# Kernel optimization log

Hardware: AMD Instinct MI355X
Metric: run time of the kernel (lower is better)

Reference implementation:

```python
import jax, jax.numpy as jnp
import numpy as np

N = 100000   # nodes
E = 3200000  # directed edges
EPS = 1e-5   # batchnorm eps


def setup_inputs() -> dict:
    key = jax.random.key(0)
    ks = jax.random.split(key, 12)
    x = jax.random.normal(ks[0], (N, 128), jnp.float32)
    edge_index = jax.random.randint(ks[1], (2, E), 0, N, dtype=jnp.int32).astype(jnp.int64)
    W1 = jax.random.normal(ks[2], (128, 256), jnp.float32) * (1.0 / np.sqrt(128))
    W2 = jax.random.normal(ks[3], (256, 256), jnp.float32) * (1.0 / np.sqrt(256))
    W3 = jax.random.normal(ks[4], (256, 40), jnp.float32) * (1.0 / np.sqrt(256))
    return {
        "x": x, "edge_index": edge_index,
        "W1": W1, "b1": jnp.zeros((256,), jnp.float32),
        "W2": W2, "b2": jnp.zeros((256,), jnp.float32),
        "W3": W3, "b3": jnp.zeros((40,), jnp.float32),
        "g1": jnp.ones((256,), jnp.float32), "be1": jnp.zeros((256,), jnp.float32),
        "g2": jnp.ones((256,), jnp.float32), "be2": jnp.zeros((256,), jnp.float32),
    }


def _gcn_conv(x, src, dst, norm, W, b):
    # GCNConv: transform then normalized sparse aggregation (A_hat @ (x W)) + b
    h = x @ W                              # [N, F_out]
    msg = h[src] * norm[:, None]           # gather + edge scaling, [E+N, F_out]
    return jax.ops.segment_sum(msg, dst, num_segments=N) + b


def _bn(h, g, b):
    # BatchNorm over the node dimension (batch stats, biased variance)
    m = h.mean(axis=0)
    v = h.var(axis=0)
    return (h - m) * jax.lax.rsqrt(v + EPS) * g + b


def reference(x, edge_index, W1, b1, W2, b2, W3, b3, g1, be1, g2, be2):
    # add self-loops (A + I), symmetric degree normalization D^-1/2 (A+I) D^-1/2
    loop = jnp.arange(N, dtype=edge_index.dtype)
    src = jnp.concatenate([edge_index[0], loop])
    dst = jnp.concatenate([edge_index[1], loop])
    deg = jax.ops.segment_sum(jnp.ones_like(src, jnp.float32), dst, num_segments=N)
    dinv = jax.lax.rsqrt(jnp.maximum(deg, 1.0))
    norm = dinv[src] * dinv[dst]           # [E+N]

    h = _gcn_conv(x, src, dst, norm, W1, b1)
    h = jax.nn.relu(_bn(h, g1, be1))       # dropout: identity (eval mode)
    h = _gcn_conv(h, src, dst, norm, W2, b2)
    h = jax.nn.relu(_bn(h, g2, be2))
    h = _gcn_conv(h, src, dst, norm, W3, b3)
    return jax.nn.log_softmax(h, axis=1)
```

## Files before the change

kernel.cpp:

```cpp
#include <hip/hip_runtime.h>
#include <hip/hip_bf16.h>
#include <math.h>

#define NNODES 100000
#define NEDGES 3200000
#define BN_EPS 1e-5f
#define NCH 391

typedef unsigned int uint;
typedef unsigned short ushort;
typedef __attribute__((ext_vector_type(8))) short bf16x8;
typedef __attribute__((ext_vector_type(4))) float f32x4;

__device__ inline float bflo(uint u) { return __uint_as_float(u << 16); }
__device__ inline float bfhi(uint u) { return __uint_as_float(u & 0xffff0000u); }
__device__ inline ushort f2bf(float f) {
    __hip_bfloat16 h = __float2bfloat16(f);
    union { __hip_bfloat16 b; ushort u; } c; c.b = h; return c.u;
}


__global__ void k_hist(const int* __restrict__ dst, int* __restrict__ cnt) {
    int e = (blockIdx.x * 256 + threadIdx.x) * 2;
    int2 v = *(const int2*)(dst + e);
    atomicAdd(&cnt[v.x], 1);
    atomicAdd(&cnt[v.y], 1);
}

__global__ void k_deg(const int* __restrict__ cnt, float* __restrict__ dinv,
                      int* __restrict__ chunksums) {
    __shared__ int s[256];
    int i = blockIdx.x * 256 + threadIdx.x;
    int c = (i < NNODES) ? cnt[i] : 0;
    if (i < NNODES) dinv[i] = rsqrtf((float)c + 1.0f);
    s[threadIdx.x] = c;
    __syncthreads();
    for (int o = 128; o > 0; o >>= 1) {
        if (threadIdx.x < o) s[threadIdx.x] += s[threadIdx.x + o];
        __syncthreads();
    }
    if (threadIdx.x == 0) chunksums[blockIdx.x] = s[0];
}

__global__ void k_scan1(int* __restrict__ chunksums, int* __restrict__ rowstart) {
    __shared__ int s[512];
    int t = threadIdx.x;
    int v = (t < NCH) ? chunksums[t] : 0;
    s[t] = v;
    __syncthreads();
    for (int o = 1; o < 512; o <<= 1) {
        int add = (t >= o) ? s[t - o] : 0;
        __syncthreads();
        s[t] += add;
        __syncthreads();
    }
    if (t < NCH) chunksums[t] = s[t] - v;
    if (t == NCH - 1) rowstart[NNODES] = s[t];
}

__global__ void k_scan2(const int* __restrict__ cnt, const int* __restrict__ chunkbase,
                        int* __restrict__ rowstart, int* __restrict__ cursor) {
    __shared__ int s[256];
    int t = threadIdx.x;
    int i = blockIdx.x * 256 + t;
    int v = (i < NNODES) ? cnt[i] : 0;
    s[t] = v;
    __syncthreads();
    for (int o = 1; o < 256; o <<= 1) {
        int add = (t >= o) ? s[t - o] : 0;
        __syncthreads();
        s[t] += add;
        __syncthreads();
    }
    if (i < NNODES) {
        int excl = s[t] - v + chunkbase[blockIdx.x];
        rowstart[i] = excl;
        cursor[i]   = excl;
    }
}

__global__ void k_scatter(const int* __restrict__ src, const int* __restrict__ dst,
                          const float* __restrict__ dinv, int* __restrict__ cursor,
                          int2* __restrict__ pairs) {
    int e = blockIdx.x * 256 + threadIdx.x;
    if (e >= NEDGES) return;
    int s = src[e], d = dst[e];
    int p = atomicAdd(&cursor[d], 1);
    float w = dinv[s] * dinv[d];
    pairs[p] = make_int2(s, __float_as_int(w));
}


template <int F, int U>
__global__ __launch_bounds__(256) void k_aggh(
    const ushort* __restrict__ X, ushort* __restrict__ Y,
    const int2* __restrict__ pairs, const int* __restrict__ rowstart,
    const float* __restrict__ dinv) {
    constexpr int CPL = F / 32;
    const int wv = threadIdx.x >> 6;
    const int lane = threadIdx.x & 63;
    const int h = lane >> 5, l32 = lane & 31;
    const int d = blockIdx.x * 4 + wv;
    const int r0 = rowstart[d], r1 = rowstart[d + 1];
    const ushort* Xb = X + (size_t)CPL * l32;
    float acc[CPL] = {};
    int p = r0;
    for (; p + 2 * U <= r1; p += 2 * U) {
        int2 e[U];
#pragma unroll
        for (int j = 0; j < U; ++j) e[j] = pairs[p + 2 * j + h];
        if constexpr (CPL == 8) {
            uint4 u[U];
#pragma unroll
            for (int j = 0; j < U; ++j) u[j] = *(const uint4*)(Xb + (size_t)e[j].x * F);
#pragma unroll
            for (int j = 0; j < U; ++j) {
                float w = __int_as_float(e[j].y);
                acc[0]=fmaf(w,bflo(u[j].x),acc[0]); acc[1]=fmaf(w,bfhi(u[j].x),acc[1]);
                acc[2]=fmaf(w,bflo(u[j].y),acc[2]); acc[3]=fmaf(w,bfhi(u[j].y),acc[3]);
                acc[4]=fmaf(w,bflo(u[j].z),acc[4]); acc[5]=fmaf(w,bfhi(u[j].z),acc[5]);
                acc[6]=fmaf(w,bflo(u[j].w),acc[6]); acc[7]=fmaf(w,bfhi(u[j].w),acc[7]);
            }
        } else {
            uint2 u[U];
#pragma unroll
            for (int j = 0; j < U; ++j) u[j] = *(const uint2*)(Xb + (size_t)e[j].x * F);
#pragma unroll
            for (int j = 0; j < U; ++j) {
                float w = __int_as_float(e[j].y);
                acc[0]=fmaf(w,bflo(u[j].x),acc[0]); acc[1]=fmaf(w,bfhi(u[j].x),acc[1]);
                acc[2]=fmaf(w,bflo(u[j].y),acc[2]); acc[3]=fmaf(w,bfhi(u[j].y),acc[3]);
            }
        }
    }
    for (; p + 2 <= r1; p += 2) {
        int2 e = pairs[p + h];
        float w = __int_as_float(e.y);
        if constexpr (CPL == 8) {
            uint4 u = *(const uint4*)(Xb + (size_t)e.x * F);
            acc[0]=fmaf(w,bflo(u.x),acc[0]); acc[1]=fmaf(w,bfhi(u.x),acc[1]);
            acc[2]=fmaf(w,bflo(u.y),acc[2]); acc[3]=fmaf(w,bfhi(u.y),acc[3]);
            acc[4]=fmaf(w,bflo(u.z),acc[4]); acc[5]=fmaf(w,bfhi(u.z),acc[5]);
            acc[6]=fmaf(w,bflo(u.w),acc[6]); acc[7]=fmaf(w,bfhi(u.w),acc[7]);
        } else {
            uint2 u = *(const uint2*)(Xb + (size_t)e.x * F);
            acc[0]=fmaf(w,bflo(u.x),acc[0]); acc[1]=fmaf(w,bfhi(u.x),acc[1]);
            acc[2]=fmaf(w,bflo(u.y),acc[2]); acc[3]=fmaf(w,bfhi(u.y),acc[3]);
        }
    }
    if (p < r1 && h == 0) {
        int2 e = pairs[p];
        float w = __int_as_float(e.y);
        if constexpr (CPL == 8) {
            uint4 u = *(const uint4*)(Xb + (size_t)e.x * F);
            acc[0]=fmaf(w,bflo(u.x),acc[0]); acc[1]=fmaf(w,bfhi(u.x),acc[1]);
            acc[2]=fmaf(w,bflo(u.y),acc[2]); acc[3]=fmaf(w,bfhi(u.y),acc[3]);
            acc[4]=fmaf(w,bflo(u.z),acc[4]); acc[5]=fmaf(w,bfhi(u.z),acc[5]);
            acc[6]=fmaf(w,bflo(u.w),acc[6]); acc[7]=fmaf(w,bfhi(u.w),acc[7]);
        } else {
            uint2 u = *(const uint2*)(Xb + (size_t)e.x * F);
            acc[0]=fmaf(w,bflo(u.x),acc[0]); acc[1]=fmaf(w,bfhi(u.x),acc[1]);
            acc[2]=fmaf(w,bflo(u.y),acc[2]); acc[3]=fmaf(w,bfhi(u.y),acc[3]);
        }
    }
#pragma unroll
    for (int c = 0; c < CPL; ++c) acc[c] += __shfl_xor(acc[c], 32);
    if (h == 0) {
        float di = dinv[d], ws = di * di;
        if constexpr (CPL == 8) {
            uint4 u = *(const uint4*)(Xb + (size_t)d * F);
            acc[0]=fmaf(ws,bflo(u.x),acc[0]); acc[1]=fmaf(ws,bfhi(u.x),acc[1]);
            acc[2]=fmaf(ws,bflo(u.y),acc[2]); acc[3]=fmaf(ws,bfhi(u.y),acc[3]);
            acc[4]=fmaf(ws,bflo(u.z),acc[4]); acc[5]=fmaf(ws,bfhi(u.z),acc[5]);
            acc[6]=fmaf(ws,bflo(u.w),acc[6]); acc[7]=fmaf(ws,bfhi(u.w),acc[7]);
            uint4 o;
            o.x = (uint)f2bf(acc[0]) | ((uint)f2bf(acc[1]) << 16);
            o.y = (uint)f2bf(acc[2]) | ((uint)f2bf(acc[3]) << 16);
            o.z = (uint)f2bf(acc[4]) | ((uint)f2bf(acc[5]) << 16);
            o.w = (uint)f2bf(acc[6]) | ((uint)f2bf(acc[7]) << 16);
            *(uint4*)(Y + (size_t)d * F + CPL * l32) = o;
        } else {
            uint2 u = *(const uint2*)(Xb + (size_t)d * F);
            acc[0]=fmaf(ws,bflo(u.x),acc[0]); acc[1]=fmaf(ws,bfhi(u.x),acc[1]);
            acc[2]=fmaf(ws,bflo(u.y),acc[2]); acc[3]=fmaf(ws,bfhi(u.y),acc[3]);
            uint2 o;
            o.x = (uint)f2bf(acc[0]) | ((uint)f2bf(acc[1]) << 16);
            o.y = (uint)f2bf(acc[2]) | ((uint)f2bf(acc[3]) << 16);
            *(uint2*)(Y + (size_t)d * F + CPL * l32) = o;
        }
    }
}


__global__ __launch_bounds__(256) void k_agg40lsm(
    const ushort* __restrict__ X, float* __restrict__ out,
    const int2* __restrict__ pairs, const int* __restrict__ rowstart,
    const float* __restrict__ dinv, const float* __restrict__ bias) {
    int t = threadIdx.x;
    int wid = t >> 6, lane = t & 63;
    int sub = lane >> 5, l32 = lane & 31;
    int d = blockIdx.x * 8 + wid * 2 + sub;
    bool act = l32 < 20;
    int col = act ? 2 * l32 : 0;
    const int r0 = rowstart[d], r1 = rowstart[d + 1];
    float a0 = 0.f, a1 = 0.f;
    int p = r0;
    for (; p + 8 <= r1; p += 8) {
        int2 e[8]; uint u[8];
#pragma unroll
        for (int j = 0; j < 8; ++j) e[j] = pairs[p + j];
#pragma unroll
        for (int j = 0; j < 8; ++j) u[j] = *(const uint*)(X + (size_t)e[j].x * 40 + col);
#pragma unroll
        for (int j = 0; j < 8; ++j) {
            float w = __int_as_float(e[j].y);
            a0 = fmaf(w, bflo(u[j]), a0); a1 = fmaf(w, bfhi(u[j]), a1);
        }
    }
    for (; p < r1; ++p) {
        int2 e = pairs[p];
        uint u = *(const uint*)(X + (size_t)e.x * 40 + col);
        float w_ = __int_as_float(e.y);
        a0 = fmaf(w_, bflo(u), a0); a1 = fmaf(w_, bfhi(u), a1);
    }
    float di = dinv[d], ws = di * di;
    uint us = *(const uint*)(X + (size_t)d * 40 + col);
    a0 = fmaf(ws, bflo(us), a0); a1 = fmaf(ws, bfhi(us), a1);
    if (act) { a0 += bias[col]; a1 += bias[col + 1]; }
    else     { a0 = -INFINITY;  a1 = -INFINITY; }
    float mx = fmaxf(a0, a1);
    for (int o = 16; o > 0; o >>= 1) mx = fmaxf(mx, __shfl_xor(mx, o, 32));
    float e = act ? (expf(a0 - mx) + expf(a1 - mx)) : 0.f;
    float s = e;
    for (int o = 16; o > 0; o >>= 1) s += __shfl_xor(s, o, 32);
    float ls = logf(s);
    if (act)
        *(float2*)(out + (size_t)d * 40 + col) = make_float2(a0 - mx - ls, a1 - mx - ls);
}


__global__ void k_xtobf16(const float* __restrict__ X, ushort* __restrict__ O) {
    int i = blockIdx.x * 256 + threadIdx.x;
    float4 v = ((const float4*)X)[i];
    ushort4 o; o.x=f2bf(v.x); o.y=f2bf(v.y); o.z=f2bf(v.z); o.w=f2bf(v.w);
    ((ushort4*)O)[i] = o;
}

__global__ void k_wconv3(const float* __restrict__ W1, const float* __restrict__ W2,
                         const float* __restrict__ W3, ushort* __restrict__ W1t,
                         ushort* __restrict__ W2t, ushort* __restrict__ W3t) {
    int b = blockIdx.x;
    if (b < 256) {
        int n = b;
        for (int k = threadIdx.x; k < 128; k += 256)
            W1t[n * 128 + k] = f2bf(W1[(size_t)k * 256 + n]);
    } else if (b < 512) {
        int n = b - 256;
        for (int k = threadIdx.x; k < 256; k += 256)
            W2t[n * 256 + k] = f2bf(W2[(size_t)k * 256 + n]);
    } else {
        int n = b - 512;
        for (int k = threadIdx.x; k < 256; k += 256)
            W3t[n * 256 + k] = (n < 40) ? f2bf(W3[(size_t)k * 40 + n]) : (ushort)0;
    }
}


__device__ inline bf16x8 bnrelu8(bf16x8 v, const float* __restrict__ scsh, int ch) {
    bf16x8 r;
#pragma unroll
    for (int j = 0; j < 8; ++j) {
        float f = __uint_as_float(((uint)(ushort)v[j]) << 16);
        f = fmaxf(fmaf(f, scsh[ch + j], scsh[256 + ch + j]), 0.f);
        r[j] = (short)f2bf(f);
    }
    return r;
}

template <int K, bool BNA, bool STATS>
__global__ __launch_bounds__(256) void k_gmm(
    const ushort* __restrict__ A, const ushort* __restrict__ Bt,
    const float* __restrict__ scsh, ushort* __restrict__ C,
    float* __restrict__ sums) {
    __shared__ ushort As[128 * 32];
    __shared__ ushort Bs[128 * 32];
    const int m0 = blockIdx.x * 128;
    const int n0 = blockIdx.y * 128;
    const int tid = threadIdx.x;
    const int lane = tid & 63;
    const int wid = tid >> 6;
    const int wr = wid >> 1, wc = wid & 1;
    const int sr1 = tid >> 2, sc = tid & 3;
    const int sr2 = sr1 + 64;
    const int ssl1 = sr1 * 32 + ((sc ^ ((sr1 >> 1) & 3)) * 8);
    const int ssl2 = sr2 * 32 + ((sc ^ ((sr2 >> 1) & 3)) * 8);
    const size_t ga1 = (size_t)min(m0 + sr1, NNODES - 1) * K + sc * 8;
    const size_t ga2 = (size_t)min(m0 + sr2, NNODES - 1) * K + sc * 8;
    const size_t gb1 = (size_t)(n0 + sr1) * K + sc * 8;
    const size_t gb2 = (size_t)(n0 + sr2) * K + sc * 8;
    const int kc = lane >> 4, rr = lane & 15;
    f32x4 acc[4][4] = {};
    for (int k0 = 0; k0 < K; k0 += 32) {
        bf16x8 av1 = *(const bf16x8*)(A + ga1 + k0);
        bf16x8 av2 = *(const bf16x8*)(A + ga2 + k0);
        bf16x8 bv1 = *(const bf16x8*)(Bt + gb1 + k0);
        bf16x8 bv2 = *(const bf16x8*)(Bt + gb2 + k0);
        if constexpr (BNA) {
            int ch = k0 + sc * 8;
            av1 = bnrelu8(av1, scsh, ch);
            av2 = bnrelu8(av2, scsh, ch);
        }
        if (k0) __syncthreads();
        *(bf16x8*)(As + ssl1) = av1;
        *(bf16x8*)(As + ssl2) = av2;
        *(bf16x8*)(Bs + ssl1) = bv1;
        *(bf16x8*)(Bs + ssl2) = bv2;
        __syncthreads();
        bf16x8 af[4], bfr[4];
#pragma unroll
        for (int f = 0; f < 4; ++f) {
            int ar = wr * 64 + f * 16 + rr;
            int br = wc * 64 + f * 16 + rr;
            af[f]  = *(const bf16x8*)(As + ar * 32 + ((kc ^ ((ar >> 1) & 3)) * 8));
            bfr[f] = *(const bf16x8*)(Bs + br * 32 + ((kc ^ ((br >> 1) & 3)) * 8));
        }
#pragma unroll
        for (int fm = 0; fm < 4; ++fm)
#pragma unroll
            for (int fn = 0; fn < 4; ++fn)
                acc[fm][fn] = __builtin_amdgcn_mfma_f32_16x16x32_bf16(af[fm], bfr[fn], acc[fm][fn], 0, 0, 0);
    }
    const int crow0 = m0 + wr * 64 + (lane >> 4) * 4;
    const int ccol0 = n0 + wc * 64 + (lane & 15);
#pragma unroll
    for (int fm = 0; fm < 4; ++fm) {
#pragma unroll
        for (int r = 0; r < 4; ++r) {
            int m = crow0 + fm * 16 + r;
            if (m >= NNODES) continue;
#pragma unroll
            for (int fn = 0; fn < 4; ++fn)
                C[(size_t)m * 256 + ccol0 + fn * 16] = f2bf(acc[fm][fn][r]);
        }
    }
    if constexpr (STATS) {
#pragma unroll
        for (int fn = 0; fn < 4; ++fn) {
            float s = 0.f, s2 = 0.f;
#pragma unroll
            for (int fm = 0; fm < 4; ++fm)
#pragma unroll
                for (int r = 0; r < 4; ++r) {
                    int m = crow0 + fm * 16 + r;
                    if (m < NNODES) { float v = acc[fm][fn][r]; s += v; s2 += v * v; }
                }
            s  += __shfl_xor(s, 16);  s  += __shfl_xor(s, 32);
            s2 += __shfl_xor(s2, 16); s2 += __shfl_xor(s2, 32);
            if (lane < 16) {
                int ch = ccol0 + fn * 16;
                atomicAdd(&sums[ch], s);
                atomicAdd(&sums[256 + ch], s2);
            }
        }
    }
}


__global__ __launch_bounds__(256) void k_gmm3m(
    const ushort* __restrict__ A, const ushort* __restrict__ Bt,
    const float* __restrict__ scsh, ushort* __restrict__ C) {
    __shared__ ushort As[128 * 64];
    __shared__ ushort Bs[48 * 64];
    const int m0 = blockIdx.x * 128;
    const int tid = threadIdx.x;
    const int lane = tid & 63;
    const int wm = tid >> 6;
    const int kc = lane >> 4, rr = lane & 15;
    f32x4 acc[2][3] = {};
    for (int k0 = 0; k0 < 256; k0 += 64) {
        bf16x8 avs[4];
        int arow[4], ach[4];
#pragma unroll
        for (int i = 0; i < 4; ++i) {
            int c = i * 256 + tid;
            arow[i] = c >> 3; ach[i] = c & 7;
            int m = min(m0 + arow[i], NNODES - 1);
            bf16x8 v = *(const bf16x8*)(A + (size_t)m * 256 + k0 + ach[i] * 8);
            avs[i] = bnrelu8(v, scsh, k0 + ach[i] * 8);
        }
        bf16x8 bvs[2];
#pragma unroll
        for (int i = 0; i < 2; ++i) {
            int c = i * 256 + tid;
            if (c < 384) {
                int row = c >> 3, ch = c & 7;
                bvs[i] = *(const bf16x8*)(Bt + (size_t)row * 256 + k0 + ch * 8);
            }
        }
        if (k0) __syncthreads();
#pragma unroll
        for (int i = 0; i < 4; ++i)
            *(bf16x8*)(As + arow[i] * 64 + ((ach[i] ^ (arow[i] & 7)) * 8)) = avs[i];
#pragma unroll
        for (int i = 0; i < 2; ++i) {
            int c = i * 256 + tid;
            if (c < 384) {
                int row = c >> 3, ch = c & 7;
                *(bf16x8*)(Bs + row * 64 + ((ch ^ (row & 7)) * 8)) = bvs[i];
            }
        }
        __syncthreads();
#pragma unroll
        for (int ks = 0; ks < 2; ++ks) {
            bf16x8 af[2], bfm[3];
#pragma unroll
            for (int fm = 0; fm < 2; ++fm) {
                int ar = wm * 32 + fm * 16 + rr;
                af[fm] = *(const bf16x8*)(As + ar * 64 + (((ks * 4 + kc) ^ (ar & 7)) * 8));
            }
#pragma unroll
            for (int fn = 0; fn < 3; ++fn) {
                int br = fn * 16 + rr;
                bfm[fn] = *(const bf16x8*)(Bs + br * 64 + (((ks * 4 + kc) ^ (br & 7)) * 8));
            }
#pragma unroll
            for (int fm = 0; fm < 2; ++fm)
#pragma unroll
                for (int fn = 0; fn < 3; ++fn)
                    acc[fm][fn] = __builtin_amdgcn_mfma_f32_16x16x32_bf16(af[fm], bfm[fn], acc[fm][fn], 0, 0, 0);
        }
    }
    const int crow0 = m0 + wm * 32 + (lane >> 4) * 4;
    const int ccol = lane & 15;
#pragma unroll
    for (int fm = 0; fm < 2; ++fm)
#pragma unroll
        for (int r = 0; r < 4; ++r) {
            int m = crow0 + fm * 16 + r;
            if (m >= NNODES) continue;
#pragma unroll
            for (int fn = 0; fn < 3; ++fn) {
                int col = fn * 16 + ccol;
                if (col < 40) C[(size_t)m * 40 + col] = f2bf(acc[fm][fn][r]);
            }
        }
}


__global__ void k_bnstats_bf(const uint* __restrict__ H, float* __restrict__ sums) {
    int t = threadIdx.x;
    int pp = t & 127, half = t >> 7;
    size_t row0 = (size_t)blockIdx.x * 256 + half * 128;
    float s0=0, s20=0, s1=0, s21=0;
    for (int i = 0; i < 128; ++i) {
        size_t m = row0 + i;
        if (m >= NNODES) break;
        uint u = H[m * 128 + pp];
        float v0 = bflo(u), v1 = bfhi(u);
        s0 += v0; s20 += v0*v0; s1 += v1; s21 += v1*v1;
    }
    atomicAdd(&sums[2*pp],       s0);
    atomicAdd(&sums[2*pp+1],     s1);
    atomicAdd(&sums[256+2*pp],   s20);
    atomicAdd(&sums[256+2*pp+1], s21);
}

__global__ void k_bnfin(const float* __restrict__ sums, const float* __restrict__ g,
                        const float* __restrict__ be, float* __restrict__ scsh) {
    int c = threadIdx.x;
    float mean = sums[c] * (1.0f / NNODES);
    float var  = sums[256 + c] * (1.0f / NNODES) - mean * mean;
    float sc = g[c] * rsqrtf(var + BN_EPS);
    scsh[c] = sc;
    scsh[256 + c] = be[c] - mean * sc;
}


extern "C" void kernel_launch(void* const* d_in, const int* in_sizes, int n_in,
                              void* d_out, int out_size, void* d_ws, size_t ws_size,
                              hipStream_t stream) {
    const float* x  = (const float*)d_in[0];
    const int*   ei = (const int*)d_in[1];
    const float* W1 = (const float*)d_in[2];
    const float* W2 = (const float*)d_in[4];
    const float* W3 = (const float*)d_in[6];
    const float* b3 = (const float*)d_in[7];
    const float* g1 = (const float*)d_in[8];
    const float* be1 = (const float*)d_in[9];
    const float* g2 = (const float*)d_in[10];
    const float* be2 = (const float*)d_in[11];
    float* out = (float*)d_out;

    const int* esrc = ei;
    const int* edst = ei + NEDGES;

    char* p = (char*)d_ws;
    auto alloc = [&](size_t bytes) { char* r = p; p += (bytes + 511) & ~(size_t)511; return r; };
    float* dinv     = (float*)alloc((size_t)NNODES * 4);
    int*   cnt      = (int*)  alloc((size_t)NNODES * 4);
    int*   rowstart = (int*)  alloc((size_t)(NNODES + 1) * 4);
    int*   cursor   = (int*)  alloc((size_t)NNODES * 4);
    int*   chunksums= (int*)  alloc((size_t)NCH * 4);
    float* stats    = (float*)alloc((size_t)2048 * 4);
    ushort* W1t     = (ushort*)alloc((size_t)256 * 128 * 2);
    ushort* W2t     = (ushort*)alloc((size_t)256 * 256 * 2);
    ushort* W3t     = (ushort*)alloc((size_t)48 * 256 * 2);
    int2*  pairs    = (int2*) alloc((size_t)NEDGES * 8);
    char*  R1       = alloc((size_t)NNODES * 256 * 2);
    char*  R2       = alloc((size_t)NNODES * 256 * 2);
    char*  R3       = alloc((size_t)NNODES * 256 * 2);

    ushort* xbf16 = (ushort*)R1;
    ushort* P_bf  = (ushort*)R1 + (size_t)NNODES * 128;
    ushort* t3_bf = (ushort*)R1;
    ushort* h1_bf = (ushort*)R2;
    ushort* h2_bf = (ushort*)R2;
    ushort* t_bf  = (ushort*)R3;

    float* sums1 = stats;        float* scsh1 = stats + 512;
    float* sums2 = stats + 1024; float* scsh2 = stats + 1536;

    hipMemsetAsync(cnt, 0, (size_t)NNODES * 4, stream);
    hipMemsetAsync(stats, 0, (size_t)2048 * 4, stream);

    k_hist<<<NEDGES / 512, 256, 0, stream>>>(edst, cnt);
    k_deg<<<NCH, 256, 0, stream>>>(cnt, dinv, chunksums);
    k_scan1<<<1, 512, 0, stream>>>(chunksums, rowstart);
    k_scan2<<<NCH, 256, 0, stream>>>(cnt, chunksums, rowstart, cursor);
    k_scatter<<<NEDGES / 256, 256, 0, stream>>>(esrc, edst, dinv, cursor, pairs);

    k_wconv3<<<560, 256, 0, stream>>>(W1, W2, W3, W1t, W2t, W3t);
    k_xtobf16<<<NNODES * 128 / 4 / 256, 256, 0, stream>>>(x, xbf16);

    dim3 ggrid((NNODES + 127) / 128, 2);

    k_aggh<128, 8><<<NNODES / 4, 256, 0, stream>>>(xbf16, P_bf, pairs, rowstart, dinv);
    k_gmm<128, false, true><<<ggrid, 256, 0, stream>>>(P_bf, W1t, nullptr, h1_bf, sums1);
    k_bnfin<<<1, 256, 0, stream>>>(sums1, g1, be1, scsh1);

    k_gmm<256, true, false><<<ggrid, 256, 0, stream>>>(h1_bf, W2t, scsh1, t_bf, nullptr);
    k_aggh<256, 8><<<NNODES / 4, 256, 0, stream>>>(t_bf, h2_bf, pairs, rowstart, dinv);
    k_bnstats_bf<<<NCH, 256, 0, stream>>>((const uint*)h2_bf, sums2);
    k_bnfin<<<1, 256, 0, stream>>>(sums2, g2, be2, scsh2);

    k_gmm3m<<<(NNODES + 127) / 128, 256, 0, stream>>>(h2_bf, W3t, scsh2, t3_bf);
    k_agg40lsm<<<NNODES / 8, 256, 0, stream>>>(t3_bf, out, pairs, rowstart, dinv, b3);
}
```

Baseline: 942.1 us.

## Two-pass bucketed CSR scatter, fuse setup kernels, fold BN finalize into GEMMs

The single-pass edge scatter, which does random atomics and writes into a 100K-node CSR, becomes a two-pass scheme. The first pass bins edges into 256-node buckets using per-bucket cursors and packs the low destination bits with the source index. The second pass scatters each bucket locally, so the writes and atomics stay cache-friendly. The histogram, x-to-bf16 and weight conversion kernels are merged into one launch, and the BatchNorm finalize step is recomputed per block inside the consuming GEMMs to remove two tiny launches. This adds an extra pass over 3.2M edges, a temporary buffer that reuses R3, and redundant per-block BN math.

Measured after the change: 1.941 ms. 106% more time.

```diff
diff --git a/kernel.cpp b/kernel.cpp
--- a/kernel.cpp
+++ b/kernel.cpp
@@ -20,11 +20,37 @@
 }
 
 
-__global__ void k_hist(const int* __restrict__ dst, int* __restrict__ cnt) {
-    int e = (blockIdx.x * 256 + threadIdx.x) * 2;
-    int2 v = *(const int2*)(dst + e);
-    atomicAdd(&cnt[v.x], 1);
-    atomicAdd(&cnt[v.y], 1);
+__global__ void k_setup(const int* __restrict__ edst, int* __restrict__ cnt,
+                        const float* __restrict__ x, ushort* __restrict__ xbf16,
+                        const float* __restrict__ W1, const float* __restrict__ W2,
+                        const float* __restrict__ W3, ushort* __restrict__ W1t,
+                        ushort* __restrict__ W2t, ushort* __restrict__ W3t) {
+    int b = blockIdx.x;
+    if (b < 6250) {
+        int e = (b * 256 + threadIdx.x) * 2;
+        int2 v = *(const int2*)(edst + e);
+        atomicAdd(&cnt[v.x], 1);
+        atomicAdd(&cnt[v.y], 1);
+    } else if (b < 18750) {
+        int i = (b - 6250) * 256 + threadIdx.x;
+        float4 v = ((const float4*)x)[i];
+        ushort4 o; o.x=f2bf(v.x); o.y=f2bf(v.y); o.z=f2bf(v.z); o.w=f2bf(v.w);
+        ((ushort4*)xbf16)[i] = o;
+    } else {
+        int bb = b - 18750;
+        if (bb < 256) {
+            for (int k = threadIdx.x; k < 128; k += 256)
+                W1t[bb * 128 + k] = f2bf(W1[(size_t)k * 256 + bb]);
+        } else if (bb < 512) {
+            int n = bb - 256;
+            for (int k = threadIdx.x; k < 256; k += 256)
+                W2t[n * 256 + k] = f2bf(W2[(size_t)k * 256 + n]);
+        } else {
+            int n = bb - 512;
+            for (int k = threadIdx.x; k < 256; k += 256)
+                W3t[n * 256 + k] = (n < 40) ? f2bf(W3[(size_t)k * 40 + n]) : (ushort)0;
+        }
+    }
 }
 
 __global__ void k_deg(const int* __restrict__ cnt, float* __restrict__ dinv,
@@ -42,7 +68,8 @@
     if (threadIdx.x == 0) chunksums[blockIdx.x] = s[0];
 }
 
-__global__ void k_scan1(int* __restrict__ chunksums, int* __restrict__ rowstart) {
+__global__ void k_scan1(int* __restrict__ chunksums, int* __restrict__ rowstart,
+                        int* __restrict__ bcursor) {
     __shared__ int s[512];
     int t = threadIdx.x;
     int v = (t < NCH) ? chunksums[t] : 0;
@@ -54,7 +81,7 @@
         s[t] += add;
         __syncthreads();
     }
-    if (t < NCH) chunksums[t] = s[t] - v;
+    if (t < NCH) { int ex = s[t] - v; chunksums[t] = ex; bcursor[t] = ex; }
     if (t == NCH - 1) rowstart[NNODES] = s[t];
 }
 
@@ -79,15 +106,36 @@
     }
 }
 
-__global__ void k_scatter(const int* __restrict__ src, const int* __restrict__ dst,
-                          const float* __restrict__ dinv, int* __restrict__ cursor,
-                          int2* __restrict__ pairs) {
-    int e = blockIdx.x * 256 + threadIdx.x;
-    if (e >= NEDGES) return;
-    int s = src[e], d = dst[e];
-    int p = atomicAdd(&cursor[d], 1);
-    float w = dinv[s] * dinv[d];
-    pairs[p] = make_int2(s, __float_as_int(w));
+
+__global__ void k_scatA(const int* __restrict__ src, const int* __restrict__ dst,
+                        const float* __restrict__ dinv, int* __restrict__ bcursor,
+                        int2* __restrict__ tmp) {
+    int e = (blockIdx.x * 256 + threadIdx.x) * 2;
+    int2 ss = *(const int2*)(src + e);
+    int2 dd = *(const int2*)(dst + e);
+#pragma unroll
+    for (int j = 0; j < 2; ++j) {
+        int s = j ? ss.y : ss.x, d = j ? dd.y : dd.x;
+        int pos = atomicAdd(&bcursor[d >> 8], 1);
+        float w = dinv[s] * dinv[d];
+        tmp[pos] = make_int2(s | ((d & 255) << 17), __float_as_int(w));
+    }
+}
+
+__global__ void k_scatB(const int* __restrict__ chunkbase, const int2* __restrict__ tmp,
+                        int* __restrict__ cursor, int2* __restrict__ pairs) {
+    int b = blockIdx.x >> 1, h = blockIdx.x & 1;
+    int start = chunkbase[b];
+    int end = (b == NCH - 1) ? NEDGES : chunkbase[b + 1];
+    int mid = (start + end) >> 1;
+    int lo = h ? mid : start, hi = h ? end : mid;
+    for (int i = lo + threadIdx.x; i < hi; i += 256) {
+        int2 t = tmp[i];
+        int s = t.x & 0x1FFFF;
+        int d = (b << 8) | (t.x >> 17);
+        int pos = atomicAdd(&cursor[d], 1);
+        pairs[pos] = make_int2(s, t.y);
+    }
 }
 
 
@@ -239,34 +287,7 @@
 }
 
 
-__global__ void k_xtobf16(const float* __restrict__ X, ushort* __restrict__ O) {
-    int i = blockIdx.x * 256 + threadIdx.x;
-    float4 v = ((const float4*)X)[i];
-    ushort4 o; o.x=f2bf(v.x); o.y=f2bf(v.y); o.z=f2bf(v.z); o.w=f2bf(v.w);
-    ((ushort4*)O)[i] = o;
-}
-
-__global__ void k_wconv3(const float* __restrict__ W1, const float* __restrict__ W2,
-                         const float* __restrict__ W3, ushort* __restrict__ W1t,
-                         ushort* __restrict__ W2t, ushort* __restrict__ W3t) {
-    int b = blockIdx.x;
-    if (b < 256) {
-        int n = b;
-        for (int k = threadIdx.x; k < 128; k += 256)
-            W1t[n * 128 + k] = f2bf(W1[(size_t)k * 256 + n]);
-    } else if (b < 512) {
-        int n = b - 256;
-        for (int k = threadIdx.x; k < 256; k += 256)
-            W2t[n * 256 + k] = f2bf(W2[(size_t)k * 256 + n]);
-    } else {
-        int n = b - 512;
-        for (int k = threadIdx.x; k < 256; k += 256)
-            W3t[n * 256 + k] = (n < 40) ? f2bf(W3[(size_t)k * 40 + n]) : (ushort)0;
-    }
-}
-
-
-__device__ inline bf16x8 bnrelu8(bf16x8 v, const float* __restrict__ scsh, int ch) {
+__device__ inline bf16x8 bnrelu8(bf16x8 v, const float* scsh, int ch) {
     bf16x8 r;
 #pragma unroll
     for (int j = 0; j < 8; ++j) {
@@ -280,24 +301,35 @@
 template <int K, bool BNA, bool STATS>
 __global__ __launch_bounds__(256) void k_gmm(
     const ushort* __restrict__ A, const ushort* __restrict__ Bt,
-    const float* __restrict__ scsh, ushort* __restrict__ C,
-    float* __restrict__ sums) {
+    const float* __restrict__ bsums, const float* __restrict__ g,
+    const float* __restrict__ be, ushort* __restrict__ C,
+    float* __restrict__ sums_out) {
     __shared__ ushort As[128 * 32];
     __shared__ ushort Bs[128 * 32];
+    __shared__ float scsh[512];
+    if constexpr (BNA) {
+        int c = threadIdx.x;
+        float mean = bsums[c] * (1.0f / NNODES);
+        float var  = bsums[256 + c] * (1.0f / NNODES) - mean * mean;
+        float sc = g[c] * rsqrtf(var + BN_EPS);
+        scsh[c] = sc;
+        scsh[256 + c] = be[c] - mean * sc;
+        __syncthreads();
+    }
     const int m0 = blockIdx.x * 128;
     const int n0 = blockIdx.y * 128;
     const int tid = threadIdx.x;
     const int lane = tid & 63;
     const int wid = tid >> 6;
     const int wr = wid >> 1, wc = wid & 1;
-    const int sr1 = tid >> 2, sc = tid & 3;
+    const int sr1 = tid >> 2, sc_ = tid & 3;
     const int sr2 = sr1 + 64;
-    const int ssl1 = sr1 * 32 + ((sc ^ ((sr1 >> 1) & 3)) * 8);
-    const int ssl2 = sr2 * 32 + ((sc ^ ((sr2 >> 1) & 3)) * 8);
-    const size_t ga1 = (size_t)min(m0 + sr1, NNODES - 1) * K + sc * 8;
-    const size_t ga2 = (size_t)min(m0 + sr2, NNODES - 1) * K + sc * 8;
-    const size_t gb1 = (size_t)(n0 + sr1) * K + sc * 8;
-    const size_t gb2 = (size_t)(n0 + sr2) * K + sc * 8;
+    const int ssl1 = sr1 * 32 + ((sc_ ^ ((sr1 >> 1) & 3)) * 8);
+    const int ssl2 = sr2 * 32 + ((sc_ ^ ((sr2 >> 1) & 3)) * 8);
+    const size_t ga1 = (size_t)min(m0 + sr1, NNODES - 1) * K + sc_ * 8;
+    const size_t ga2 = (size_t)min(m0 + sr2, NNODES - 1) * K + sc_ * 8;
+    const size_t gb1 = (size_t)(n0 + sr1) * K + sc_ * 8;
+    const size_t gb2 = (size_t)(n0 + sr2) * K + sc_ * 8;
     const int kc = lane >> 4, rr = lane & 15;
     f32x4 acc[4][4] = {};
     for (int k0 = 0; k0 < K; k0 += 32) {
@@ -306,7 +338,7 @@
         bf16x8 bv1 = *(const bf16x8*)(Bt + gb1 + k0);
         bf16x8 bv2 = *(const bf16x8*)(Bt + gb2 + k0);
         if constexpr (BNA) {
-            int ch = k0 + sc * 8;
+            int ch = k0 + sc_ * 8;
             av1 = bnrelu8(av1, scsh, ch);
             av2 = bnrelu8(av2, scsh, ch);
         }
@@ -358,8 +390,8 @@
             s2 += __shfl_xor(s2, 16); s2 += __shfl_xor(s2, 32);
             if (lane < 16) {
                 int ch = ccol0 + fn * 16;
-                atomicAdd(&sums[ch], s);
-                atomicAdd(&sums[256 + ch], s2);
+                atomicAdd(&sums_out[ch], s);
+                atomicAdd(&sums_out[256 + ch], s2);
             }
         }
     }
@@ -368,9 +400,20 @@
 
 __global__ __launch_bounds__(256) void k_gmm3m(
     const ushort* __restrict__ A, const ushort* __restrict__ Bt,
-    const float* __restrict__ scsh, ushort* __restrict__ C) {
+    const float* __restrict__ bsums, const float* __restrict__ g,
+    const float* __restrict__ be, ushort* __restrict__ C) {
     __shared__ ushort As[128 * 64];
     __shared__ ushort Bs[48 * 64];
+    __shared__ float scsh[512];
+    {
+        int c = threadIdx.x;
+        float mean = bsums[c] * (1.0f / NNODES);
+        float var  = bsums[256 + c] * (1.0f / NNODES) - mean * mean;
+        float sc = g[c] * rsqrtf(var + BN_EPS);
+        scsh[c] = sc;
+        scsh[256 + c] = be[c] - mean * sc;
+        __syncthreads();
+    }
     const int m0 = blockIdx.x * 128;
     const int tid = threadIdx.x;
     const int lane = tid & 63;
@@ -463,16 +506,6 @@
     atomicAdd(&sums[2*pp+1],     s1);
     atomicAdd(&sums[256+2*pp],   s20);
     atomicAdd(&sums[256+2*pp+1], s21);
-}
-
-__global__ void k_bnfin(const float* __restrict__ sums, const float* __restrict__ g,
-                        const float* __restrict__ be, float* __restrict__ scsh) {
-    int c = threadIdx.x;
-    float mean = sums[c] * (1.0f / NNODES);
-    float var  = sums[256 + c] * (1.0f / NNODES) - mean * mean;
-    float sc = g[c] * rsqrtf(var + BN_EPS);
-    scsh[c] = sc;
-    scsh[256 + c] = be[c] - mean * sc;
 }
 
 
@@ -501,6 +534,7 @@
     int*   rowstart = (int*)  alloc((size_t)(NNODES + 1) * 4);
     int*   cursor   = (int*)  alloc((size_t)NNODES * 4);
     int*   chunksums= (int*)  alloc((size_t)NCH * 4);
+    int*   bcursor  = (int*)  alloc((size_t)NCH * 4);
     float* stats    = (float*)alloc((size_t)2048 * 4);
     ushort* W1t     = (ushort*)alloc((size_t)256 * 128 * 2);
     ushort* W2t     = (ushort*)alloc((size_t)256 * 256 * 2);
@@ -515,34 +549,31 @@
     ushort* t3_bf = (ushort*)R1;
     ushort* h1_bf = (ushort*)R2;
     ushort* h2_bf = (ushort*)R2;
+    int2*   tmp   = (int2*)R3;
     ushort* t_bf  = (ushort*)R3;
 
-    float* sums1 = stats;        float* scsh1 = stats + 512;
-    float* sums2 = stats + 1024; float* scsh2 = stats + 1536;
+    float* sums1 = stats;
+    float* sums2 = stats + 1024;
 
     hipMemsetAsync(cnt, 0, (size_t)NNODES * 4, stream);
     hipMemsetAsync(stats, 0, (size_t)2048 * 4, stream);
 
-    k_hist<<<NEDGES / 512, 256, 0, stream>>>(edst, cnt);
+    k_setup<<<19310, 256, 0, stream>>>(edst, cnt, x, xbf16, W1, W2, W3, W1t, W2t, W3t);
     k_deg<<<NCH, 256, 0, stream>>>(cnt, dinv, chunksums);
-    k_scan1<<<1, 512, 0, stream>>>(chunksums, rowstart);
+    k_scan1<<<1, 512, 0, stream>>>(chunksums, rowstart, bcursor);
     k_scan2<<<NCH, 256, 0, stream>>>(cnt, chunksums, rowstart, cursor);
-    k_scatter<<<NEDGES / 256, 256, 0, stream>>>(esrc, edst, dinv, cursor, pairs);
-
-    k_wconv3<<<560, 256, 0, stream>>>(W1, W2, W3, W1t, W2t, W3t);
-    k_xtobf16<<<NNODES * 128 / 4 / 256, 256, 0, stream>>>(x, xbf16);
+    k_scatA<<<NEDGES / 512, 256, 0, stream>>>(esrc, edst, dinv, bcursor, tmp);
+    k_scatB<<<NCH * 2, 256, 0, stream>>>(chunksums, tmp, cursor, pairs);
 
     dim3 ggrid((NNODES + 127) / 128, 2);
 
     k_aggh<128, 8><<<NNODES / 4, 256, 0, stream>>>(xbf16, P_bf, pairs, rowstart, dinv);
-    k_gmm<128, false, true><<<ggrid, 256, 0, stream>>>(P_bf, W1t, nullptr, h1_bf, sums1);
-    k_bnfin<<<1, 256, 0, stream>>>(sums1, g1, be1, scsh1);
-
-    k_gmm<256, true, false><<<ggrid, 256, 0, stream>>>(h1_bf, W2t, scsh1, t_bf, nullptr);
+    k_gmm<128, false, true><<<ggrid, 256, 0, stream>>>(P_bf, W1t, nullptr, nullptr, nullptr, h1_bf, sums1);
+
+    k_gmm<256, true, false><<<ggrid, 256, 0, stream>>>(h1_bf, W2t, sums1, g1, be1, t_bf, nullptr);
     k_aggh<256, 8><<<NNODES / 4, 256, 0, stream>>>(t_bf, h2_bf, pairs, rowstart, dinv);
     k_bnstats_bf<<<NCH, 256, 0, stream>>>((const uint*)h2_bf, sums2);
-    k_bnfin<<<1, 256, 0, stream>>>(sums2, g2, be2, scsh2);
-
-    k_gmm3m<<<(NNODES + 127) / 128, 256, 0, stream>>>(h2_bf, W3t, scsh2, t3_bf);
+
+    k_gmm3m<<<(NNODES + 127) / 128, 256, 0, stream>>>(h2_bf, W3t, sums2, g2, be2, t3_bf);
     k_agg40lsm<<<NNODES / 8, 256, 0, stream>>>(t3_bf, out, pairs, rowstart, dinv, b3);
 }
```
